# Kernel optimization log

Measured on AMD Instinct MI355X. Metric: run time of the kernel, lower is better.

Reference implementation:

```python
import jax, jax.numpy as jnp
import numpy as np

N_NODES = 200000
N_EDGES = 400000
IN_CH, HID_CH, OUT_CH = 768, 256, 256
NUM_GRAPHS = 8000


def setup_inputs() -> dict:
    key = jax.random.key(0)
    k = jax.random.split(key, 8)
    x = jax.random.normal(k[0], (N_NODES, IN_CH), dtype=jnp.float32)
    edge_index = jax.random.randint(k[1], (2, N_EDGES), 0, N_NODES, dtype=jnp.int64)
    batch = jnp.sort(jax.random.randint(k[2], (N_NODES,), 0, NUM_GRAPHS, dtype=jnp.int64))
    # GCNConv params (Glorot-ish scale)
    W1 = jax.random.normal(k[3], (IN_CH, HID_CH), dtype=jnp.float32) / np.sqrt(IN_CH)
    b1 = jnp.zeros((HID_CH,), dtype=jnp.float32)
    W2 = jax.random.normal(k[4], (HID_CH, OUT_CH), dtype=jnp.float32) / np.sqrt(HID_CH)
    b2 = jnp.zeros((OUT_CH,), dtype=jnp.float32)
    return {"x": x, "W1": W1, "b1": b1, "W2": W2, "b2": b2,
            "edge_index": edge_index, "batch": batch}


def gcn_conv(x, W, b, src, dst, norm):
    # PyG GCNConv: linear transform, then normalized gather-scatter aggregation
    h = x @ W  # [N, C_out]
    msg = h[src] * norm[:, None]  # gather + scale, [E_sl, C_out]
    out = jax.ops.segment_sum(msg, dst, num_segments=N_NODES)  # scatter-add
    return out + b


def reference(x, W1, b1, W2, b2, edge_index, batch):
    # Add self-loops (PyG GCNConv default add_self_loops=True)
    loops = jnp.arange(N_NODES, dtype=edge_index.dtype)
    src = jnp.concatenate([edge_index[0], loops])
    dst = jnp.concatenate([edge_index[1], loops])
    # Symmetric degree normalization: deg computed on dst (incl. self-loops)
    deg = jax.ops.segment_sum(jnp.ones_like(dst, dtype=x.dtype), dst, num_segments=N_NODES)
    dinv = jnp.where(deg > 0, jax.lax.rsqrt(deg), 0.0)
    norm = dinv[src] * dinv[dst]  # [E_sl]

    h = gcn_conv(x, W1, b1, src, dst, norm)
    h = jax.nn.relu(h)
    h = gcn_conv(h, W2, b2, src, dst, norm)

    # global_mean_pool over batch vector
    sums = jax.ops.segment_sum(h, batch, num_segments=NUM_GRAPHS)
    counts = jax.ops.segment_sum(jnp.ones((N_NODES,), dtype=h.dtype), batch, num_segments=NUM_GRAPHS)
    return sums / jnp.maximum(counts, 1.0)[:, None]
```

## Files before the change

kernel.cpp:

```cpp
#include <hip/hip_runtime.h>


#define N_NODES_C 200000
#define N_EDGES_C 400000
#define IN_CH_C 768
#define HID_C 256
#define NUM_GRAPHS_C 8000

typedef __attribute__((ext_vector_type(8))) short short8;
typedef __attribute__((ext_vector_type(4))) float f32x4;

__device__ __forceinline__ unsigned short f2bf(float f) {
  union { float f; unsigned u; } v; v.f = f;
  unsigned r = v.u + 0x7FFFu + ((v.u >> 16) & 1u);
  return (unsigned short)(r >> 16);
}


__global__ void zero2_kernel(int* __restrict__ a, int* __restrict__ b, int n) {
  int i = blockIdx.x * blockDim.x + threadIdx.x;
  if (i < n) { a[i] = 0; b[i] = 0; }
}

__global__ void hist_kernel(const int* __restrict__ dst, int* __restrict__ deg, int E) {
  int e = blockIdx.x * blockDim.x + threadIdx.x;
  if (e < E) atomicAdd(&deg[dst[e]], 1);
}

__global__ void dinv_kernel(const int* __restrict__ deg, float* __restrict__ dinv, int n) {
  int i = blockIdx.x * blockDim.x + threadIdx.x;
  if (i < n) dinv[i] = rsqrtf((float)(deg[i] + 1));
}

__global__ __launch_bounds__(256) void scan1_kernel(const int* __restrict__ deg,
                                                    int* __restrict__ offs,
                                                    int* __restrict__ bsums, int n) {
  __shared__ int s[256];
  int tid = threadIdx.x;
  int i = blockIdx.x * 256 + tid;
  int v = (i < n) ? deg[i] : 0;
  s[tid] = v;
  __syncthreads();
  for (int d = 1; d < 256; d <<= 1) {
    int t = (tid >= d) ? s[tid - d] : 0;
    __syncthreads();
    s[tid] += t;
    __syncthreads();
  }
  if (i < n) offs[i] = s[tid] - v;
  if (tid == 255) bsums[blockIdx.x] = s[255];
}

__global__ __launch_bounds__(1024) void scan2_kernel(int* __restrict__ bsums, int nb) {
  __shared__ int s[1024];
  int tid = threadIdx.x;
  int v = (tid < nb) ? bsums[tid] : 0;
  s[tid] = v;
  __syncthreads();
  for (int d = 1; d < 1024; d <<= 1) {
    int t = (tid >= d) ? s[tid - d] : 0;
    __syncthreads();
    s[tid] += t;
    __syncthreads();
  }
  if (tid < nb) bsums[tid] = s[tid] - v;
}

__global__ void scan3_kernel(int* __restrict__ offs, const int* __restrict__ bsums, int n) {
  int i = blockIdx.x * 256 + threadIdx.x;
  if (i < n) offs[i] += bsums[blockIdx.x];
  if (i == 0) offs[n] = N_EDGES_C;
}

__global__ void scatter_kernel(const int* __restrict__ esrc_in, const int* __restrict__ edst_in,
                               const int* __restrict__ offs, int* __restrict__ cursor,
                               const float* __restrict__ dinv,
                               int* __restrict__ esrc, float* __restrict__ enorm, int E) {
  int e = blockIdx.x * blockDim.x + threadIdx.x;
  if (e >= E) return;
  int s = esrc_in[e], d = edst_in[e];
  int pos = offs[d] + atomicAdd(&cursor[d], 1);
  esrc[pos] = s;
  enorm[pos] = dinv[s] * dinv[d];
}


__global__ void wprep_kernel(const float* __restrict__ W, unsigned short* __restrict__ WT,
                             int K, int N, int total) {
  int idx = blockIdx.x * blockDim.x + threadIdx.x;
  if (idx >= total) return;
  int n = idx / K, k = idx - n * K;
  WT[idx] = f2bf(W[(size_t)k * N + n]);
}


#define BM 128
#define BN 128
#define BK 32
#define LDT 40

__global__ __launch_bounds__(256) void gemm_bf16_kernel(
    const float* __restrict__ A, const unsigned short* __restrict__ BT,
    float* __restrict__ C, int M, int K) {
  __shared__ unsigned short As[BM * LDT];
  __shared__ unsigned short Bs[BN * LDT];
  const int tid = threadIdx.x;
  const int row0 = blockIdx.y * BM;
  const int col0 = blockIdx.x * BN;
  const int lane = tid & 63;
  const int w = tid >> 6;
  const int wm = (w >> 1) * 64, wn = (w & 1) * 64;
  const int r16 = lane & 15, quad = lane >> 4;

  f32x4 acc[4][4] = {};

  const int srow = tid >> 1;
  const int sk = (tid & 1) * 16;

  for (int k0 = 0; k0 < K; k0 += BK) {
    {
      const int gr = row0 + srow;
      float vals[16];
      if (gr < M) {
        const float* ap = &A[(size_t)gr * K + k0 + sk];
#pragma unroll
        for (int i = 0; i < 4; ++i) *(float4*)&vals[i * 4] = *(const float4*)&ap[i * 4];
      } else {
#pragma unroll
        for (int i = 0; i < 16; ++i) vals[i] = 0.f;
      }
      unsigned short hb[16];
#pragma unroll
      for (int i = 0; i < 16; ++i) hb[i] = f2bf(vals[i]);
      *(uint4*)&As[srow * LDT + sk] = *(uint4*)&hb[0];
      *(uint4*)&As[srow * LDT + sk + 8] = *(uint4*)&hb[8];
    }
    {
      const unsigned short* bp = &BT[(size_t)(col0 + srow) * K + k0 + sk];
      uint4 v0 = *(const uint4*)&bp[0];
      uint4 v1 = *(const uint4*)&bp[8];
      *(uint4*)&Bs[srow * LDT + sk] = v0;
      *(uint4*)&Bs[srow * LDT + sk + 8] = v1;
    }
    __syncthreads();

    short8 af[4], bfr[4];
#pragma unroll
    for (int i = 0; i < 4; ++i)
      af[i] = *(const short8*)&As[(wm + i * 16 + r16) * LDT + quad * 8];
#pragma unroll
    for (int j = 0; j < 4; ++j)
      bfr[j] = *(const short8*)&Bs[(wn + j * 16 + r16) * LDT + quad * 8];
#pragma unroll
    for (int i = 0; i < 4; ++i)
#pragma unroll
      for (int j = 0; j < 4; ++j)
        acc[i][j] = __builtin_amdgcn_mfma_f32_16x16x32_bf16(af[i], bfr[j], acc[i][j], 0, 0, 0);
    __syncthreads();
  }

#pragma unroll
  for (int i = 0; i < 4; ++i) {
#pragma unroll
    for (int r = 0; r < 4; ++r) {
      int gr = row0 + wm + i * 16 + quad * 4 + r;
      if (gr < M) {
#pragma unroll
        for (int j = 0; j < 4; ++j)
          C[(size_t)gr * HID_C + col0 + wn + j * 16 + r16] = acc[i][j][r];
      }
    }
  }
}


__global__ __launch_bounds__(256) void aggregate_kernel(
    const float* __restrict__ t, float* __restrict__ out,
    const int* __restrict__ offs, const int* __restrict__ esrc,
    const float* __restrict__ enorm, const float* __restrict__ dinv,
    const float* __restrict__ bias, int do_relu) {
  int wid = (int)(((unsigned)blockIdx.x * blockDim.x + threadIdx.x) >> 6);
  int lane = threadIdx.x & 63;
  if (wid >= N_NODES_C) return;
  int node = wid;
  float di = dinv[node];
  float sn = di * di;
  const float4 tv = *(const float4*)&t[(size_t)node * HID_C + lane * 4];
  float4 acc = make_float4(tv.x * sn, tv.y * sn, tv.z * sn, tv.w * sn);
  int beg = offs[node], end = offs[node + 1];
  for (int p = beg; p < end; ++p) {
    int s = esrc[p];
    float w = enorm[p];
    const float4 v = *(const float4*)&t[(size_t)s * HID_C + lane * 4];
    acc.x += v.x * w; acc.y += v.y * w; acc.z += v.z * w; acc.w += v.w * w;
  }
  const float4 bv = *(const float4*)&bias[lane * 4];
  acc.x += bv.x; acc.y += bv.y; acc.z += bv.z; acc.w += bv.w;
  if (do_relu) {
    acc.x = fmaxf(acc.x, 0.f); acc.y = fmaxf(acc.y, 0.f);
    acc.z = fmaxf(acc.z, 0.f); acc.w = fmaxf(acc.w, 0.f);
  }
  *(float4*)&out[(size_t)node * HID_C + lane * 4] = acc;
}


__device__ __forceinline__ int lower_bound_dev(const int* __restrict__ a, int n, int key) {
  int lo = 0, hi = n;
  while (lo < hi) {
    int mid = (lo + hi) >> 1;
    if (a[mid] < key) lo = mid + 1; else hi = mid;
  }
  return lo;
}

__global__ __launch_bounds__(256) void pool_kernel(const float* __restrict__ h,
                                                   const int* __restrict__ batch,
                                                   float* __restrict__ out) {
  int wid = (int)(((unsigned)blockIdx.x * blockDim.x + threadIdx.x) >> 6);
  int lane = threadIdx.x & 63;
  if (wid >= NUM_GRAPHS_C) return;
  int g = wid;
  int lo = lower_bound_dev(batch, N_NODES_C, g);
  int hi = lower_bound_dev(batch, N_NODES_C, g + 1);
  float4 acc = make_float4(0.f, 0.f, 0.f, 0.f);
  for (int i = lo; i < hi; ++i) {
    const float4 v = *(const float4*)&h[(size_t)i * HID_C + lane * 4];
    acc.x += v.x; acc.y += v.y; acc.z += v.z; acc.w += v.w;
  }
  float inv = 1.0f / fmaxf((float)(hi - lo), 1.0f);
  acc.x *= inv; acc.y *= inv; acc.z *= inv; acc.w *= inv;
  *(float4*)&out[(size_t)g * HID_C + lane * 4] = acc;
}


extern "C" void kernel_launch(void* const* d_in, const int* in_sizes, int n_in,
                              void* d_out, int out_size, void* d_ws, size_t ws_size,
                              hipStream_t stream) {
  (void)in_sizes; (void)n_in; (void)out_size; (void)ws_size;
  const float* x  = (const float*)d_in[0];
  const float* W1 = (const float*)d_in[1];
  const float* b1 = (const float*)d_in[2];
  const float* W2 = (const float*)d_in[3];
  const float* b2 = (const float*)d_in[4];
  const int* edge_index = (const int*)d_in[5];
  const int* batch = (const int*)d_in[6];
  const int* e_src = edge_index;
  const int* e_dst = edge_index + N_EDGES_C;
  float* out = (float*)d_out;

  float* t      = (float*)d_ws;
  float* h      = t + (size_t)N_NODES_C * HID_C;
  float* dinv   = h + (size_t)N_NODES_C * HID_C;
  int*   deg    = (int*)(dinv + N_NODES_C);
  int*   offs   = deg + N_NODES_C;
  int*   cursor = offs + (N_NODES_C + 64);
  int*   esrc   = cursor + N_NODES_C;
  float* enorm  = (float*)(esrc + N_EDGES_C);
  int*   bsums  = (int*)(enorm + N_EDGES_C);
  unsigned short* W1T = (unsigned short*)cursor;
  unsigned short* W2T = W1T + (size_t)IN_CH_C * HID_C;

  const int NB = (N_NODES_C + 255) / 256;
  const int EB = (N_EDGES_C + 255) / 256;

  zero2_kernel<<<NB, 256, 0, stream>>>(deg, cursor, N_NODES_C);
  hist_kernel<<<EB, 256, 0, stream>>>(e_dst, deg, N_EDGES_C);
  scan1_kernel<<<NB, 256, 0, stream>>>(deg, offs, bsums, N_NODES_C);
  scan2_kernel<<<1, 1024, 0, stream>>>(bsums, NB);
  scan3_kernel<<<NB, 256, 0, stream>>>(offs, bsums, N_NODES_C);
  dinv_kernel<<<NB, 256, 0, stream>>>(deg, dinv, N_NODES_C);
  scatter_kernel<<<EB, 256, 0, stream>>>(e_src, e_dst, offs, cursor, dinv, esrc, enorm, N_EDGES_C);

  wprep_kernel<<<(IN_CH_C * HID_C + 255) / 256, 256, 0, stream>>>(W1, W1T, IN_CH_C, HID_C, IN_CH_C * HID_C);
  wprep_kernel<<<(HID_C * HID_C + 255) / 256, 256, 0, stream>>>(W2, W2T, HID_C, HID_C, HID_C * HID_C);

  dim3 g1(HID_C / BN, (N_NODES_C + BM - 1) / BM);
  gemm_bf16_kernel<<<g1, 256, 0, stream>>>(x, W1T, t, N_NODES_C, IN_CH_C);
  aggregate_kernel<<<(N_NODES_C * 64 + 255) / 256, 256, 0, stream>>>(
      t, h, offs, esrc, enorm, dinv, b1, 1);
  gemm_bf16_kernel<<<g1, 256, 0, stream>>>(h, W2T, t, N_NODES_C, HID_C);
  aggregate_kernel<<<(N_NODES_C * 64 + 255) / 256, 256, 0, stream>>>(
      t, h, offs, esrc, enorm, dinv, b2, 0);
  pool_kernel<<<(NUM_GRAPHS_C * 64 + 255) / 256, 256, 0, stream>>>(h, batch, out);
}
```

Measured before the change: 1.391 ms.

## Widen GEMM tile to full output width and prefetch next K-slice into registers

The GEMM block now covers all 256 output columns with 512 threads (8 waves), so each row block of A is read from global memory once instead of twice. The main loop also loads the next K-slice of A and B into registers while MFMAs run on the current LDS tile, overlapping global-memory latency with compute. In exchange, register pressure per thread and LDS per block go up, and there are half as many blocks, which may lower occupancy.

Result: faster. 1.362 ms (-2.1%).

```diff
diff --git a/kernel.cpp b/kernel.cpp
--- a/kernel.cpp
+++ b/kernel.cpp
@@ -95,54 +95,64 @@
 
 
 #define BM 128
-#define BN 128
+#define BN 256
 #define BK 32
 #define LDT 40
 
-__global__ __launch_bounds__(256) void gemm_bf16_kernel(
+__global__ __launch_bounds__(512) void gemm_bf16_kernel(
     const float* __restrict__ A, const unsigned short* __restrict__ BT,
     float* __restrict__ C, int M, int K) {
   __shared__ unsigned short As[BM * LDT];
   __shared__ unsigned short Bs[BN * LDT];
   const int tid = threadIdx.x;
-  const int row0 = blockIdx.y * BM;
-  const int col0 = blockIdx.x * BN;
+  const int row0 = blockIdx.x * BM;
   const int lane = tid & 63;
   const int w = tid >> 6;
-  const int wm = (w >> 1) * 64, wn = (w & 1) * 64;
+  const int wm = (w >> 2) * 64;
+  const int wn = (w & 3) * 64;
   const int r16 = lane & 15, quad = lane >> 4;
 
   f32x4 acc[4][4] = {};
 
-  const int srow = tid >> 1;
-  const int sk = (tid & 1) * 16;
+  const int arow = tid >> 2;
+  const int ak = (tid & 3) * 8;
+  const int brow = tid >> 1;
+  const int bk = (tid & 1) * 16;
+
+  const bool avalid = (row0 + arow) < M;
+  const float* aptr = &A[(size_t)(row0 + arow) * K + ak];
+  const unsigned short* bptr = &BT[(size_t)brow * K + bk];
+
+  float av[8];
+  uint4 bv0, bv1;
+  if (avalid) {
+    *(float4*)&av[0] = *(const float4*)&aptr[0];
+    *(float4*)&av[4] = *(const float4*)&aptr[4];
+  } else {
+#pragma unroll
+    for (int i = 0; i < 8; ++i) av[i] = 0.f;
+  }
+  bv0 = *(const uint4*)&bptr[0];
+  bv1 = *(const uint4*)&bptr[8];
 
   for (int k0 = 0; k0 < K; k0 += BK) {
     {
-      const int gr = row0 + srow;
-      float vals[16];
-      if (gr < M) {
-        const float* ap = &A[(size_t)gr * K + k0 + sk];
-#pragma unroll
-        for (int i = 0; i < 4; ++i) *(float4*)&vals[i * 4] = *(const float4*)&ap[i * 4];
-      } else {
-#pragma unroll
-        for (int i = 0; i < 16; ++i) vals[i] = 0.f;
+      unsigned short hb[8];
+#pragma unroll
+      for (int i = 0; i < 8; ++i) hb[i] = f2bf(av[i]);
+      *(uint4*)&As[arow * LDT + ak] = *(uint4*)&hb[0];
+      *(uint4*)&Bs[brow * LDT + bk] = bv0;
+      *(uint4*)&Bs[brow * LDT + bk + 8] = bv1;
+    }
+    __syncthreads();
+    if (k0 + BK < K) {
+      if (avalid) {
+        *(float4*)&av[0] = *(const float4*)&aptr[k0 + BK + 0];
+        *(float4*)&av[4] = *(const float4*)&aptr[k0 + BK + 4];
       }
-      unsigned short hb[16];
-#pragma unroll
-      for (int i = 0; i < 16; ++i) hb[i] = f2bf(vals[i]);
-      *(uint4*)&As[srow * LDT + sk] = *(uint4*)&hb[0];
-      *(uint4*)&As[srow * LDT + sk + 8] = *(uint4*)&hb[8];
+      bv0 = *(const uint4*)&bptr[k0 + BK + 0];
+      bv1 = *(const uint4*)&bptr[k0 + BK + 8];
     }
-    {
-      const unsigned short* bp = &BT[(size_t)(col0 + srow) * K + k0 + sk];
-      uint4 v0 = *(const uint4*)&bp[0];
-      uint4 v1 = *(const uint4*)&bp[8];
-      *(uint4*)&Bs[srow * LDT + sk] = v0;
-      *(uint4*)&Bs[srow * LDT + sk + 8] = v1;
-    }
-    __syncthreads();
 
     short8 af[4], bfr[4];
 #pragma unroll
@@ -167,7 +177,7 @@
       if (gr < M) {
 #pragma unroll
         for (int j = 0; j < 4; ++j)
-          C[(size_t)gr * HID_C + col0 + wn + j * 16 + r16] = acc[i][j][r];
+          C[(size_t)gr * HID_C + wn + j * 16 + r16] = acc[i][j][r];
       }
     }
   }
@@ -274,11 +284,11 @@
   wprep_kernel<<<(IN_CH_C * HID_C + 255) / 256, 256, 0, stream>>>(W1, W1T, IN_CH_C, HID_C, IN_CH_C * HID_C);
   wprep_kernel<<<(HID_C * HID_C + 255) / 256, 256, 0, stream>>>(W2, W2T, HID_C, HID_C, HID_C * HID_C);
 
-  dim3 g1(HID_C / BN, (N_NODES_C + BM - 1) / BM);
-  gemm_bf16_kernel<<<g1, 256, 0, stream>>>(x, W1T, t, N_NODES_C, IN_CH_C);
+  dim3 g1((N_NODES_C + BM - 1) / BM);
+  gemm_bf16_kernel<<<g1, 512, 0, stream>>>(x, W1T, t, N_NODES_C, IN_CH_C);
   aggregate_kernel<<<(N_NODES_C * 64 + 255) / 256, 256, 0, stream>>>(
       t, h, offs, esrc, enorm, dinv, b1, 1);
-  gemm_bf16_kernel<<<g1, 256, 0, stream>>>(h, W2T, t, N_NODES_C, HID_C);
+  gemm_bf16_kernel<<<g1, 512, 0, stream>>>(h, W2T, t, N_NODES_C, HID_C);
   aggregate_kernel<<<(N_NODES_C * 64 + 255) / 256, 256, 0, stream>>>(
       t, h, offs, esrc, enorm, dinv, b2, 0);
   pool_kernel<<<(NUM_GRAPHS_C * 64 + 255) / 256, 256, 0, stream>>>(h, batch, out);
```
